# Kernel tuning notes

Measured on AMD Instinct MI355X. Metric: run time of the kernel, lower is better.

Reference implementation:

```python
import jax, jax.numpy as jnp
import numpy as np
import math

EPS = 1e-5
GN_GROUPS = 32


def conv2d(x, w, padding):
    # x: [B,C,H,W], w: [O,I,kh,kw]
    return jax.lax.conv_general_dilated(
        x, w, window_strides=(1, 1), padding=[(padding, padding)] * 2,
        dimension_numbers=("NCHW", "OIHW", "NCHW"))


def group_norm(x, weight, bias, groups=GN_GROUPS, eps=EPS):
    B, C, H, W = x.shape
    xg = x.reshape(B, groups, C // groups, H, W)
    mu = xg.mean(axis=(2, 3, 4), keepdims=True)
    var = xg.var(axis=(2, 3, 4), keepdims=True)
    xn = (xg - mu) * jax.lax.rsqrt(var + eps)
    xn = xn.reshape(B, C, H, W)
    return xn * weight[None, :, None, None] + bias[None, :, None, None]


def setup_inputs() -> dict:
    key = jax.random.key(0)
    ks = jax.random.split(key, 8)
    B, C, H, W = 8, 256, 80, 80
    init_gate = 0.99
    gate_bias_val = 0.5 * math.log((1 + init_gate) / (1 - init_gate))
    return {
        "x": jax.random.normal(ks[0], (B, C, H, W), dtype=jnp.float32),
        "w1": jax.random.normal(ks[1], (C, C, 3, 3), dtype=jnp.float32) * 0.01,
        "gn1_w": jnp.ones((C,), dtype=jnp.float32),
        "gn1_b": jnp.zeros((C,), dtype=jnp.float32),
        "w2": jax.random.normal(ks[2], (C, C, 3, 3), dtype=jnp.float32) * 0.01,
        "gn2_w": jnp.ones((C,), dtype=jnp.float32),
        "gn2_b": jnp.zeros((C,), dtype=jnp.float32),
        "gate_w": jax.random.normal(ks[3], (1, C, 1, 1), dtype=jnp.float32) * 0.01,
        "gate_b": jnp.full((1,), gate_bias_val, dtype=jnp.float32),
    }


def reference(x, w1, gn1_w, gn1_b, w2, gn2_w, gn2_b, gate_w, gate_b):
    # shortcut is identity (in_channels == out_channels, stride 1)
    shortcut = x
    # conv1 -> GN -> ReLU
    h = jax.nn.relu(group_norm(conv2d(x, w1, padding=1), gn1_w, gn1_b))
    # conv2 -> GN
    h = group_norm(conv2d(h, w2, padding=1), gn2_w, gn2_b)
    # SpatialGate: 1x1 conv on the original input, ReTanH activation
    g = conv2d(x, gate_w, padding=0) + gate_b[None, :, None, None]  # [B,1,H,W]
    gate = jnp.clip(jnp.tanh(g), 0.0, None)
    # num_groups == 1: encode/decode are identity reshapes; gate broadcasts over C
    out = h * gate
    return jax.nn.relu(out + shortcut)
```

## Files before the change

### kernel.cpp

```cpp
#include <hip/hip_runtime.h>
#include <math.h>

#define NB   8
#define NC   256
#define NH   80
#define NW   80
#define NHW  6400
#define GN_EPS 1e-5f

typedef __bf16 bf16;
typedef bf16 bf16x2 __attribute__((ext_vector_type(2)));
typedef bf16 bf16x4 __attribute__((ext_vector_type(4)));
typedef bf16 bf16x8 __attribute__((ext_vector_type(8)));
typedef float f32x4 __attribute__((ext_vector_type(4)));

typedef __attribute__((address_space(1))) void gvoid;
typedef __attribute__((address_space(3))) void lvoid;
__device__ __forceinline__ void glds16(const void* g, void* l) {
    __builtin_amdgcn_global_load_lds((const gvoid*)g, (lvoid*)l, 16, 0, 0);
}

#define AW_Q 520
#define AW_T 2080
#define AW_BUF 18720

__global__ __launch_bounds__(256) void prep_kernel(
    const float* __restrict__ x, bf16* __restrict__ xp,
    const float* __restrict__ gw, float* __restrict__ gpart,
    const float* __restrict__ w1, const float* __restrict__ w2,
    bf16* __restrict__ wA1, bf16* __restrict__ wA2, float* __restrict__ stats)
{
    int bid = blockIdx.x;
    int tid = threadIdx.x;
    if (bid >= 20480) {
        int blk = bid - 20480;
        if (blk == 0) {
            #pragma unroll
            for (int k = 0; k < 8; k++) stats[tid + k * 256] = 0.0f;
            return;
        }
        int rb = blk - 1;
        const float* w = (rb < 2304) ? w1 : w2;
        bf16* wA       = (rb < 2304) ? wA1 : wA2;
        int idx = (rb % 2304) * 256 + tid;
        int c8 = idx & 7;
        int co = (idx >> 3) & 255;
        int qq = (idx >> 11) & 3;
        int tc = idx >> 13;
        int tap = tc % 9, chunk = tc / 9;
        int ci = chunk * 32 + qq * 8 + c8;
        wA[idx] = (bf16)w[(size_t)(co * 256 + ci) * 9 + tap];
        return;
    }
    __shared__ float tile[8 * 84];
    int row = bid % 80;
    int cib = (bid / 80) & 31;
    int b   = bid / 2560;
    for (int e = tid; e < 640; e += 256) {
        int c8 = e / 80, col = e - c8 * 80;
        tile[c8 * 84 + col] = x[((size_t)(b * NC + cib * 8 + c8) * NH + row) * NW + col];
    }
    __syncthreads();
    size_t base = (((size_t)(b * 32 + cib) * 82 + row + 1) * 82) * 8 + 8;
    for (int t = tid; t < 320; t += 256) {
        int e = 2 * t, col = e >> 3, c8 = e & 7;
        bf16x2 pk = { (bf16)tile[c8 * 84 + col], (bf16)tile[(c8 + 1) * 84 + col] };
        *(bf16x2*)(xp + base + e) = pk;
    }
    if (tid < 80) {
        int col = tid;
        float s = 0.0f;
        #pragma unroll
        for (int c8 = 0; c8 < 8; c8++) s = fmaf(tile[c8 * 84 + col], gw[cib * 8 + c8], s);
        gpart[((size_t)cib * NB + b) * NHW + row * 80 + col] = s;
    }
    const uint4 z4 = make_uint4(0u, 0u, 0u, 0u);
    size_t img = ((size_t)(b * 32 + cib)) * 82;
    if (tid < 2) {
        int col = tid * 81;
        *(uint4*)(xp + ((img + row + 1) * 82 + col) * 8) = z4;
    }
    if (row == 0 || row == 79) {
        int prow = (row == 0) ? 0 : 81;
        for (int u = tid; u < 82; u += 256)
            *(uint4*)(xp + ((img + prow) * 82 + u) * 8) = z4;
    }
}

__global__ __launch_bounds__(256, 2) void conv_kernel(
    const bf16* __restrict__ xp, const bf16* __restrict__ wA,
    bf16* __restrict__ y, float* __restrict__ ssum, float* __restrict__ ssq)
{
    __shared__ __align__(16) bf16 Aw[2 * AW_BUF];
    __shared__ float wgs[8], wgq[8];

    int tid  = threadIdx.x;
    int wid  = tid >> 6;
    int lane = tid & 63;
    int n = lane & 15, q = lane >> 4;

    int bid = blockIdx.x;
    int ct  = bid / 160;
    int t   = bid - ct * 160;
    int b   = t / 20;
    int rt  = t - b * 20;
    int co0 = ct * 64, h0 = rt * 4;

    if (tid < 8) { wgs[tid] = 0.0f; wgq[tid] = 0.0f; }

    f32x4 acc[4][5];
    #pragma unroll
    for (int i = 0; i < 4; i++)
        #pragma unroll
        for (int j = 0; j < 5; j++) acc[i][j] = (f32x4){0.f, 0.f, 0.f, 0.f};

    for (int p = wid; p < 36; p += 4) {
        int tap = p >> 2, qq = p & 3;
        glds16((const char*)(wA + ((size_t)p * 256 + co0) * 8) + lane * 16,
               (char*)(Aw + tap * AW_T + qq * AW_Q) + lane * 16);
    }

    for (int c = 0; c < 8; c++) {
        __syncthreads();
        if (c + 1 < 8) {
            bf16* dst = Aw + (((c + 1) & 1) ? AW_BUF : 0);
            for (int p = wid; p < 36; p += 4) {
                int tap = p >> 2, qq = p & 3;
                glds16((const char*)(wA + ((size_t)((c + 1) * 36 + p) * 256 + co0) * 8) + lane * 16,
                       (char*)(dst + tap * AW_T + qq * AW_Q) + lane * 16);
            }
        }
        const bf16* awc = Aw + ((c & 1) ? AW_BUF : 0) + q * AW_Q + n * 8;
        const bf16* xq = xp + (((size_t)(b * 32 + c * 4 + q) * 82 + (h0 + wid)) * 82) * 8 + n * 8;

        bf16x8 L[2][15];
        #pragma unroll
        for (int k = 0; k < 15; k++)
            L[0][k] = *(const bf16x8*)(xq + ((k / 3) * 16 + (k % 3)) * 8);
        #pragma unroll
        for (int r = 0; r < 3; r++) {
            if (r < 2) {
                #pragma unroll
                for (int k = 0; k < 15; k++)
                    L[(r + 1) & 1][k] =
                        *(const bf16x8*)(xq + ((r + 1) * 82 + (k / 3) * 16 + (k % 3)) * 8);
            }
            #pragma unroll
            for (int s = 0; s < 3; s++) {
                bf16x8 af[4];
                #pragma unroll
                for (int mt = 0; mt < 4; mt++)
                    af[mt] = *(const bf16x8*)(awc + (r * 3 + s) * AW_T + mt * 128);
                #pragma unroll
                for (int mt = 0; mt < 4; mt++)
                    #pragma unroll
                    for (int nt = 0; nt < 5; nt++)
                        acc[mt][nt] = __builtin_amdgcn_mfma_f32_16x16x32_bf16(
                            af[mt], L[r & 1][nt * 3 + s], acc[mt][nt], 0, 0, 0);
            }
        }
    }

    int h = h0 + wid;
    #pragma unroll
    for (int mt = 0; mt < 4; mt++) {
        float s1 = 0.0f, s2 = 0.0f;
        int co  = co0 + mt * 16 + q * 4;
        int cib = co >> 3, c8 = co & 7;
        #pragma unroll
        for (int nt = 0; nt < 5; nt++) {
            int col = nt * 16 + n;
            bf16x4 pk;
            #pragma unroll
            for (int rg = 0; rg < 4; rg++) {
                float v = acc[mt][nt][rg];
                pk[rg] = (bf16)v;
                s1 += v;
                s2 = fmaf(v, v, s2);
            }
            *(bf16x4*)(y + ((((size_t)(b * 32 + cib) * 80 + h) * 80 + col) * 8 + c8)) = pk;
        }
        #pragma unroll
        for (int off = 1; off < 16; off <<= 1) {
            s1 += __shfl_xor(s1, off, 64);
            s2 += __shfl_xor(s2, off, 64);
        }
        if (n == 0) {
            int gl = mt * 2 + (q >> 1);
            atomicAdd(&wgs[gl], s1);
            atomicAdd(&wgq[gl], s2);
        }
    }
    __syncthreads();
    if (tid < 8) {
        atomicAdd(&ssum[b * 32 + ct * 8 + tid], wgs[tid]);
        atomicAdd(&ssq [b * 32 + ct * 8 + tid], wgq[tid]);
    }
}

__global__ __launch_bounds__(256) void prep2_kernel(
    const bf16* __restrict__ y, bf16* __restrict__ xp,
    const float* __restrict__ s, const float* __restrict__ sq,
    const float* __restrict__ gamma, const float* __restrict__ beta,
    const float* __restrict__ gpart, const float* __restrict__ gb,
    float* __restrict__ gate)
{
    int bid = blockIdx.x;
    if (bid >= 5120) {
        int i = (bid - 5120) * 256 + threadIdx.x;
        float gs = gb[0];
        #pragma unroll 8
        for (int k = 0; k < 32; k++) gs += gpart[(size_t)k * (NB * NHW) + i];
        gate[i] = fmaxf(tanhf(gs), 0.0f);
        return;
    }
    int b = bid / 640; int rem = bid - b * 640;
    int cib = rem / 20; int rq = rem - cib * 20;
    int gidx = b * 32 + cib;
    const float cnt = (float)(8 * NHW);
    float m  = s[gidx] / cnt;
    float vv = sq[gidx] / cnt - m * m;
    float r  = rsqrtf(vv + GN_EPS);
    const bf16* src = y + (size_t)(b * 32 + cib) * 51200 + rq * 2560;
    for (int u = threadIdx.x; u < 1280; u += 256) {
        int e = 2 * u;
        int row = rq * 4 + e / 640;
        int w640 = e % 640;
        int c8 = e & 7;
        int c = cib * 8 + c8;
        float sc0 = r * gamma[c],     sh0 = beta[c]     - m * sc0;
        float sc1 = r * gamma[c + 1], sh1 = beta[c + 1] - m * sc1;
        bf16x2 iv = *(const bf16x2*)(src + e);
        bf16x2 pk = { (bf16)fmaxf(fmaf((float)iv[0], sc0, sh0), 0.0f),
                      (bf16)fmaxf(fmaf((float)iv[1], sc1, sh1), 0.0f) };
        size_t xidx = (((size_t)(b * 32 + cib) * 82 + row + 1) * 82) * 8 + 8 + w640;
        *(bf16x2*)(xp + xidx) = pk;
    }
}

__global__ __launch_bounds__(256) void final_kernel(
    const bf16* __restrict__ y, const float* __restrict__ x,
    const float* __restrict__ gate,
    const float* __restrict__ s, const float* __restrict__ sq,
    const float* __restrict__ gamma, const float* __restrict__ beta,
    float* __restrict__ out)
{
    __shared__ float lds[8 * 324];
    int bid = blockIdx.x;
    int b = bid / 640; int rem = bid - b * 640;
    int cib = rem / 20; int rq = rem - cib * 20;
    int gidx = b * 32 + cib;
    const float cnt = (float)(8 * NHW);
    float m  = s[gidx] / cnt;
    float vv = sq[gidx] / cnt - m * m;
    float r  = rsqrtf(vv + GN_EPS);
    const bf16* src = y + (size_t)(b * 32 + cib) * 51200 + rq * 2560;
    for (int u = threadIdx.x; u < 1280; u += 256) {
        int e = 2 * u;
        int c8 = e & 7;
        int rc = e >> 3;
        int c = cib * 8 + c8;
        float sc0 = r * gamma[c],     sh0 = beta[c]     - m * sc0;
        float sc1 = r * gamma[c + 1], sh1 = beta[c + 1] - m * sc1;
        bf16x2 iv = *(const bf16x2*)(src + e);
        lds[c8 * 324 + rc]       = fmaf((float)iv[0], sc0, sh0);
        lds[(c8 + 1) * 324 + rc] = fmaf((float)iv[1], sc1, sh1);
    }
    __syncthreads();
    const float* gp = gate + b * NHW + rq * 320;
    for (int e2 = threadIdx.x; e2 < 2560; e2 += 256) {
        int c8 = e2 / 320, rc = e2 - c8 * 320;
        int c = cib * 8 + c8;
        size_t oidx = (size_t)(b * NC + c) * NHW + rq * 320 + rc;
        float v = fmaf(lds[c8 * 324 + rc], gp[rc], x[oidx]);
        out[oidx] = fmaxf(v, 0.0f);
    }
}

extern "C" void kernel_launch(void* const* d_in, const int* in_sizes, int n_in,
                              void* d_out, int out_size, void* d_ws, size_t ws_size,
                              hipStream_t stream)
{
    const float* x     = (const float*)d_in[0];
    const float* w1    = (const float*)d_in[1];
    const float* gn1_w = (const float*)d_in[2];
    const float* gn1_b = (const float*)d_in[3];
    const float* w2    = (const float*)d_in[4];
    const float* gn2_w = (const float*)d_in[5];
    const float* gn2_b = (const float*)d_in[6];
    const float* gw    = (const float*)d_in[7];
    const float* gb    = (const float*)d_in[8];

    bf16*  xp    = (bf16*)d_out;
    float* gpart = (float*)((char*)d_out + 27541504);
    float* out   = (float*)d_out;

    char* wsb = (char*)d_ws;
    bf16*  y     = (bf16*)wsb;
    float* gate  = (float*)(wsb + 26214400);
    bf16*  wA1   = (bf16*)(wsb + 26214400 + 204800);
    bf16*  wA2   = wA1 + 589824;
    float* stats = (float*)(wsb + 26214400 + 204800 + 2 * 1179648);
    float* s1  = stats,        * s1q = stats + 256;
    float* s2  = stats + 1024, * s2q = stats + 1280;

    prep_kernel<<<25089, 256, 0, stream>>>(x, xp, gw, gpart, w1, w2, wA1, wA2, stats);
    conv_kernel<<<640, 256, 0, stream>>>(xp, wA1, y, s1, s1q);
    prep2_kernel<<<5320, 256, 0, stream>>>(y, xp, s1, s1q, gn1_w, gn1_b, gpart, gb, gate);
    conv_kernel<<<640, 256, 0, stream>>>(xp, wA2, y, s2, s2q);
    final_kernel<<<5120, 256, 0, stream>>>(y, x, gate, s2, s2q, gn2_w, gn2_b, out);
}
```

Before: 308.2 us.

## Batch four rows per prep block and reorder conv loads around weight prefetch

The prep kernel now processes four rows per block instead of one, cutting the block count and amortizing the per-block setup and weight-index work. In the conv kernel, the three input-row register loads are explicitly staged: rows 0 and 1 load up front, and row 2 is issued after the first tap row's MFMAs. The next chunk's weight prefetch into LDS is moved after a sched_barrier so global reads of the activations are issued before the LDS prefetch. The conv change raises register pressure (two 15-entry fragment arrays are live at once) and constrains compiler scheduling.

```diff
diff --git a/kernel.cpp b/kernel.cpp
--- a/kernel.cpp
+++ b/kernel.cpp
@@ -32,8 +32,8 @@
 {
     int bid = blockIdx.x;
     int tid = threadIdx.x;
-    if (bid >= 20480) {
-        int blk = bid - 20480;
+    if (bid >= 5120) {
+        int blk = bid - 5120;
         if (blk == 0) {
             #pragma unroll
             for (int k = 0; k < 8; k++) stats[tid + k * 256] = 0.0f;
@@ -52,36 +52,40 @@
         wA[idx] = (bf16)w[(size_t)(co * 256 + ci) * 9 + tap];
         return;
     }
-    __shared__ float tile[8 * 84];
-    int row = bid % 80;
-    int cib = (bid / 80) & 31;
-    int b   = bid / 2560;
-    for (int e = tid; e < 640; e += 256) {
-        int c8 = e / 80, col = e - c8 * 80;
-        tile[c8 * 84 + col] = x[((size_t)(b * NC + cib * 8 + c8) * NH + row) * NW + col];
+    __shared__ float tile[8][4][84];
+    int rg  = bid % 20;
+    int cib = (bid / 20) & 31;
+    int b   = bid / 640;
+    for (int e = tid; e < 2560; e += 256) {
+        int c8 = e / 320, r2 = e - c8 * 320;
+        int rr = r2 / 80, col = r2 - rr * 80;
+        tile[c8][rr][col] =
+            x[((size_t)(b * NC + cib * 8 + c8) * NH + rg * 4 + rr) * NW + col];
     }
     __syncthreads();
-    size_t base = (((size_t)(b * 32 + cib) * 82 + row + 1) * 82) * 8 + 8;
-    for (int t = tid; t < 320; t += 256) {
-        int e = 2 * t, col = e >> 3, c8 = e & 7;
-        bf16x2 pk = { (bf16)tile[c8 * 84 + col], (bf16)tile[(c8 + 1) * 84 + col] };
+    for (int t = tid; t < 1280; t += 256) {
+        int rr = t / 320, t2 = t - rr * 320;
+        int e = 2 * t2, col = e >> 3, c8 = e & 7;
+        bf16x2 pk = { (bf16)tile[c8][rr][col], (bf16)tile[c8 + 1][rr][col] };
+        size_t base = (((size_t)(b * 32 + cib) * 82 + rg * 4 + rr + 1) * 82) * 8 + 8;
         *(bf16x2*)(xp + base + e) = pk;
     }
-    if (tid < 80) {
-        int col = tid;
+    if (tid < 320) {
+        int rr = tid / 80, col = tid - rr * 80;
         float s = 0.0f;
         #pragma unroll
-        for (int c8 = 0; c8 < 8; c8++) s = fmaf(tile[c8 * 84 + col], gw[cib * 8 + c8], s);
-        gpart[((size_t)cib * NB + b) * NHW + row * 80 + col] = s;
+        for (int c8 = 0; c8 < 8; c8++)
+            s = fmaf(tile[c8][rr][col], gw[cib * 8 + c8], s);
+        gpart[((size_t)cib * NB + b) * NHW + (rg * 4 + rr) * 80 + col] = s;
     }
     const uint4 z4 = make_uint4(0u, 0u, 0u, 0u);
     size_t img = ((size_t)(b * 32 + cib)) * 82;
-    if (tid < 2) {
-        int col = tid * 81;
-        *(uint4*)(xp + ((img + row + 1) * 82 + col) * 8) = z4;
-    }
-    if (row == 0 || row == 79) {
-        int prow = (row == 0) ? 0 : 81;
+    if (tid < 8) {
+        int rr = tid >> 1, col = (tid & 1) * 81;
+        *(uint4*)(xp + ((img + rg * 4 + rr + 1) * 82 + col) * 8) = z4;
+    }
+    if (rg == 0 || rg == 19) {
+        int prow = (rg == 0) ? 0 : 81;
         for (int u = tid; u < 82; u += 256)
             *(uint4*)(xp + ((img + prow) * 82 + u) * 8) = z4;
     }
@@ -122,7 +126,37 @@
 
     for (int c = 0; c < 8; c++) {
         __syncthreads();
-        if (c + 1 < 8) {
+        const bf16* awc = Aw + ((c & 1) ? AW_BUF : 0) + q * AW_Q + n * 8;
+        const bf16* xq  = xp + (((size_t)(b * 32 + c * 4 + q) * 82 + (h0 + wid)) * 82) * 8 + n * 8;
+
+        bf16x8 L0[15], L1[15];
+        #pragma unroll
+        for (int k = 0; k < 15; k++)
+            L0[k] = *(const bf16x8*)(xq + ((k / 3) * 16 + (k % 3)) * 8);
+        #pragma unroll
+        for (int k = 0; k < 15; k++)
+            L1[k] = *(const bf16x8*)(xq + (82 + (k / 3) * 16 + (k % 3)) * 8);
+
+        #pragma unroll
+        for (int s = 0; s < 3; s++) {
+            bf16x8 af[4];
+            #pragma unroll
+            for (int mt = 0; mt < 4; mt++)
+                af[mt] = *(const bf16x8*)(awc + s * AW_T + mt * 128);
+            #pragma unroll
+            for (int mt = 0; mt < 4; mt++)
+                #pragma unroll
+                for (int nt = 0; nt < 5; nt++)
+                    acc[mt][nt] = __builtin_amdgcn_mfma_f32_16x16x32_bf16(
+                        af[mt], L0[nt * 3 + s], acc[mt][nt], 0, 0, 0);
+        }
+        #pragma unroll
+        for (int k = 0; k < 15; k++)
+            L0[k] = *(const bf16x8*)(xq + (164 + (k / 3) * 16 + (k % 3)) * 8);
+
+        __builtin_amdgcn_sched_barrier(0);
+
+        if (c < 7) {
             bf16* dst = Aw + (((c + 1) & 1) ? AW_BUF : 0);
             for (int p = wid; p < 36; p += 4) {
                 int tap = p >> 2, qq = p & 3;
@@ -130,34 +164,32 @@
                        (char*)(dst + tap * AW_T + qq * AW_Q) + lane * 16);
             }
         }
-        const bf16* awc = Aw + ((c & 1) ? AW_BUF : 0) + q * AW_Q + n * 8;
-        const bf16* xq = xp + (((size_t)(b * 32 + c * 4 + q) * 82 + (h0 + wid)) * 82) * 8 + n * 8;
-
-        bf16x8 L[2][15];
-        #pragma unroll
-        for (int k = 0; k < 15; k++)
-            L[0][k] = *(const bf16x8*)(xq + ((k / 3) * 16 + (k % 3)) * 8);
-        #pragma unroll
-        for (int r = 0; r < 3; r++) {
-            if (r < 2) {
+
+        #pragma unroll
+        for (int s = 0; s < 3; s++) {
+            bf16x8 af[4];
+            #pragma unroll
+            for (int mt = 0; mt < 4; mt++)
+                af[mt] = *(const bf16x8*)(awc + (3 + s) * AW_T + mt * 128);
+            #pragma unroll
+            for (int mt = 0; mt < 4; mt++)
                 #pragma unroll
-                for (int k = 0; k < 15; k++)
-                    L[(r + 1) & 1][k] =
-                        *(const bf16x8*)(xq + ((r + 1) * 82 + (k / 3) * 16 + (k % 3)) * 8);
-            }
-            #pragma unroll
-            for (int s = 0; s < 3; s++) {
-                bf16x8 af[4];
+                for (int nt = 0; nt < 5; nt++)
+                    acc[mt][nt] = __builtin_amdgcn_mfma_f32_16x16x32_bf16(
+                        af[mt], L1[nt * 3 + s], acc[mt][nt], 0, 0, 0);
+        }
+        #pragma unroll
+        for (int s = 0; s < 3; s++) {
+            bf16x8 af[4];
+            #pragma unroll
+            for (int mt = 0; mt < 4; mt++)
+                af[mt] = *(const bf16x8*)(awc + (6 + s) * AW_T + mt * 128);
+            #pragma unroll
+            for (int mt = 0; mt < 4; mt++)
                 #pragma unroll
-                for (int mt = 0; mt < 4; mt++)
-                    af[mt] = *(const bf16x8*)(awc + (r * 3 + s) * AW_T + mt * 128);
-                #pragma unroll
-                for (int mt = 0; mt < 4; mt++)
-                    #pragma unroll
-                    for (int nt = 0; nt < 5; nt++)
-                        acc[mt][nt] = __builtin_amdgcn_mfma_f32_16x16x32_bf16(
-                            af[mt], L[r & 1][nt * 3 + s], acc[mt][nt], 0, 0, 0);
-            }
+                for (int nt = 0; nt < 5; nt++)
+                    acc[mt][nt] = __builtin_amdgcn_mfma_f32_16x16x32_bf16(
+                        af[mt], L0[nt * 3 + s], acc[mt][nt], 0, 0, 0);
         }
     }
 
@@ -304,7 +336,7 @@
     float* s1  = stats,        * s1q = stats + 256;
     float* s2  = stats + 1024, * s2q = stats + 1280;
 
-    prep_kernel<<<25089, 256, 0, stream>>>(x, xp, gw, gpart, w1, w2, wA1, wA2, stats);
+    prep_kernel<<<9729, 256, 0, stream>>>(x, xp, gw, gpart, w1, w2, wA1, wA2, stats);
     conv_kernel<<<640, 256, 0, stream>>>(xp, wA1, y, s1, s1q);
     prep2_kernel<<<5320, 256, 0, stream>>>(y, xp, s1, s1q, gn1_w, gn1_b, gpart, gb, gate);
     conv_kernel<<<640, 256, 0, stream>>>(xp, wA2, y, s2, s2q);
```

New measurement: 299.9 us. 1.03x faster.
